# Performance work log

Hardware: AMD Instinct MI355X
Metric: run time of the kernel (lower is better)

Reference implementation:

```python
import jax, jax.numpy as jnp
import numpy as np

EPS = 1e-5

def _layernorm(x, g, b):
    mu = jnp.mean(x, axis=-1, keepdims=True)
    var = jnp.mean(jnp.square(x - mu), axis=-1, keepdims=True)
    return (x - mu) * jax.lax.rsqrt(var + EPS) * g + b

def _orthogonal(key, out_dim, in_dim):
    a = jax.random.normal(key, (max(out_dim, in_dim), min(out_dim, in_dim)), dtype=jnp.float32)
    q, r = jnp.linalg.qr(a)
    q = q * jnp.sign(jnp.diagonal(r))
    if out_dim < in_dim:
        q = q.T
    return q  # [out_dim, in_dim]

def setup_inputs() -> dict:
    key = jax.random.key(0)
    ks = jax.random.split(key, 4)
    B, OBS, H1, H2, F = 262144, 512, 128, 128, 128
    obs = jax.random.normal(ks[0], (B, OBS), dtype=jnp.float32)
    return {
        "obs": obs,
        "w1": _orthogonal(ks[1], H1, OBS), "b1": jnp.zeros((H1,), jnp.float32),
        "g1": jnp.ones((H1,), jnp.float32), "be1": jnp.zeros((H1,), jnp.float32),
        "w2": _orthogonal(ks[2], H2, H1), "b2": jnp.zeros((H2,), jnp.float32),
        "g2": jnp.ones((H2,), jnp.float32), "be2": jnp.zeros((H2,), jnp.float32),
        "w3": _orthogonal(ks[3], F, H2), "b3": jnp.zeros((F,), jnp.float32),
    }

def reference(obs, w1, b1, g1, be1, w2, b2, g2, be2, w3, b3):
    x = jnp.tanh(_layernorm(obs @ w1.T + b1, g1, be1))
    x = jnp.tanh(_layernorm(x @ w2.T + b2, g2, be2))
    return jnp.tanh(x @ w3.T + b3)
```

## Files before the change

kernel.cpp:

```cpp
#include <hip/hip_runtime.h>
#include <hip/hip_bf16.h>

typedef __attribute__((ext_vector_type(8))) __bf16 bf16x8;
typedef __attribute__((ext_vector_type(4))) float f32x4;
typedef __attribute__((ext_vector_type(8))) float f32x8;
typedef __attribute__((ext_vector_type(4))) unsigned int u32x4;

static __device__ __forceinline__ unsigned short bf16r(float f) {
  unsigned u = __builtin_bit_cast(unsigned, f);
  return (unsigned short)((u + 0x7FFFu + ((u >> 16) & 1u)) >> 16);
}

static __device__ __forceinline__ float ftanh(float x) {
  float e = __builtin_amdgcn_exp2f(x * 2.8853900817779268f);
  return 1.0f - 2.0f * __builtin_amdgcn_rcpf(e + 1.0f);
}

static __device__ __forceinline__ void gload_lds16(const void* g, void* l) {
  __builtin_amdgcn_global_load_lds(
      (const __attribute__((address_space(1))) unsigned int*)g,
      (__attribute__((address_space(3))) unsigned int*)l, 16, 0, 0);
}

__global__ void pack_kernel(const float* __restrict__ w1, const float* __restrict__ w2,
                            const float* __restrict__ w3, const float* __restrict__ b1,
                            const float* __restrict__ g1, const float* __restrict__ be1,
                            const float* __restrict__ b2, const float* __restrict__ g2,
                            const float* __restrict__ be2, const float* __restrict__ b3,
                            unsigned short* __restrict__ w1pk, unsigned short* __restrict__ w2pk,
                            unsigned short* __restrict__ w3pk, float* __restrict__ ppk) {
  int idx = blockIdx.x * 256 + threadIdx.x;
  if (idx < 65536) {
    int j = idx & 7, l = (idx >> 3) & 63, s = (idx >> 9) & 15, t = idx >> 13;
    int row = t * 16 + (l & 15);
    int col = s * 32 + (l >> 4) * 8 + j;
    w1pk[idx] = bf16r(w1[row * 512 + col]);
  } else if (idx < 81920) {
    int i = idx - 65536;
    int j = i & 7, l = (i >> 3) & 63, s = (i >> 9) & 3, t = i >> 11;
    int row = t * 16 + (l & 15);
    int col = (2 * s + (j >> 2)) * 16 + (l >> 4) * 4 + (j & 3);
    w2pk[i] = bf16r(w2[row * 128 + col]);
  } else if (idx < 98304) {
    int i = idx - 81920;
    int j = i & 7, l = (i >> 3) & 63, s = (i >> 9) & 3, t = i >> 11;
    int row = t * 16 + (l & 15);
    int col = (2 * s + (j >> 2)) * 16 + (l >> 4) * 4 + (j & 3);
    w3pk[i] = bf16r(w3[row * 128 + col]);
  } else if (idx < 99200) {
    int i = idx - 98304;
    int p = i >> 7;
    int r = i & 127;
    int qq = r >> 5, ii = r & 31;
    int m = (ii >> 2) * 16 + qq * 4 + (ii & 3);
    const float* src = (p == 0) ? b1 : (p == 1) ? g1 : (p == 2) ? be1
                     : (p == 3) ? b2 : (p == 4) ? g2 : (p == 5) ? be2 : b3;
    ppk[i] = src[m];
  }
}

__global__ __launch_bounds__(1024)
__attribute__((amdgpu_waves_per_eu(4, 4)))
void backbone_main(const float* __restrict__ obs,
                   const unsigned char* __restrict__ w1pk_g,
                   const bf16x8* __restrict__ w2pk,
                   const bf16x8* __restrict__ w3pk,
                   const float* __restrict__ ppk,
                   float* __restrict__ out) {
  __shared__ __align__(16) unsigned char w1s[131072];

  const int tid  = threadIdx.x;
  const int lane = tid & 63;
  const int wv   = tid >> 6;
  const int q    = lane >> 4;
  const int rl   = lane & 15;
  const size_t brow = (size_t)blockIdx.x * 256 + (unsigned)(wv * 16) + (unsigned)rl;

  const float* p0 = obs + brow * 512 + q * 8;

  f32x4 st[2][4];
#define LOAD_BATCH(buf, s0)                                                      \
  do {                                                                           \
    st[buf][0] = __builtin_nontemporal_load((const f32x4*)(p0 + (s0) * 32));     \
    st[buf][1] = __builtin_nontemporal_load((const f32x4*)(p0 + (s0) * 32 + 4)); \
    st[buf][2] = __builtin_nontemporal_load((const f32x4*)(p0 + (s0) * 32 + 32));\
    st[buf][3] = __builtin_nontemporal_load((const f32x4*)(p0 + (s0) * 32 + 36));\
  } while (0)

  LOAD_BATCH(0, 0);
  LOAD_BATCH(1, 2);

#pragma unroll
  for (int r = 0; r < 8; ++r) {
    gload_lds16(w1pk_g + r * 16384 + tid * 16, w1s + r * 16384 + wv * 1024);
  }
  __syncthreads();

  const bf16x8* w1l = (const bf16x8*)w1s;

  f32x4 acc[8];
#pragma unroll
  for (int t = 0; t < 8; ++t) acc[t] = (f32x4){0.f, 0.f, 0.f, 0.f};

#pragma unroll
  for (int bb = 0; bb < 8; ++bb) {
    const int cur = bb & 1;
    f32x4 a0 = st[cur][0], a1 = st[cur][1];
    f32x4 a2 = st[cur][2], a3 = st[cur][3];
    if (bb < 6) {
      LOAD_BATCH(cur, 2 * bb + 4);
    }
    f32x8 r0 = {a0.x, a0.y, a0.z, a0.w, a1.x, a1.y, a1.z, a1.w};
    f32x8 r1 = {a2.x, a2.y, a2.z, a2.w, a3.x, a3.y, a3.z, a3.w};
    bf16x8 b0 = __builtin_convertvector(r0, bf16x8);
    bf16x8 b1 = __builtin_convertvector(r1, bf16x8);
#pragma unroll
    for (int t = 0; t < 8; ++t) {
      bf16x8 af0 = w1l[(t * 16 + 2 * bb) * 64 + lane];
      acc[t] = __builtin_amdgcn_mfma_f32_16x16x32_bf16(af0, b0, acc[t], 0, 0, 0);
    }
#pragma unroll
    for (int t = 0; t < 8; ++t) {
      bf16x8 af1 = w1l[(t * 16 + 2 * bb + 1) * 64 + lane];
      acc[t] = __builtin_amdgcn_mfma_f32_16x16x32_bf16(af1, b1, acc[t], 0, 0, 0);
    }
  }
#undef LOAD_BATCH

  bf16x8 pkv[4];

  {
    const float* pb = ppk + 0 * 128 + q * 32;
    const float* pg = ppk + 1 * 128 + q * 32;
    const float* pe = ppk + 2 * 128 + q * 32;
    float s1 = 0.f, s2 = 0.f;
#pragma unroll
    for (int t = 0; t < 8; ++t) {
      f32x4 bb = *(const f32x4*)(pb + t * 4);
      f32x4 v = acc[t];
      v.x += bb.x; v.y += bb.y; v.z += bb.z; v.w += bb.w;
      acc[t] = v;
      s1 += (v.x + v.y) + (v.z + v.w);
      s2 += (v.x * v.x + v.y * v.y) + (v.z * v.z + v.w * v.w);
    }
    s1 += __shfl_xor(s1, 16, 64);
    s1 += __shfl_xor(s1, 32, 64);
    s2 += __shfl_xor(s2, 16, 64);
    s2 += __shfl_xor(s2, 32, 64);
    float mu  = s1 * (1.0f / 128.0f);
    float var = s2 * (1.0f / 128.0f) - mu * mu;
    float rs  = __builtin_amdgcn_rsqf(var + 1e-5f);
#pragma unroll
    for (int t2 = 0; t2 < 4; ++t2) {
      f32x4 ga = *(const f32x4*)(pg + (2 * t2) * 4);
      f32x4 gb = *(const f32x4*)(pg + (2 * t2 + 1) * 4);
      f32x4 ea = *(const f32x4*)(pe + (2 * t2) * 4);
      f32x4 eb = *(const f32x4*)(pe + (2 * t2 + 1) * 4);
      f32x4 va = acc[2 * t2];
      f32x4 vb = acc[2 * t2 + 1];
      f32x8 cat = {ftanh((va.x - mu) * rs * ga.x + ea.x),
                   ftanh((va.y - mu) * rs * ga.y + ea.y),
                   ftanh((va.z - mu) * rs * ga.z + ea.z),
                   ftanh((va.w - mu) * rs * ga.w + ea.w),
                   ftanh((vb.x - mu) * rs * gb.x + eb.x),
                   ftanh((vb.y - mu) * rs * gb.y + eb.y),
                   ftanh((vb.z - mu) * rs * gb.z + eb.z),
                   ftanh((vb.w - mu) * rs * gb.w + eb.w)};
      pkv[t2] = __builtin_convertvector(cat, bf16x8);
    }
  }

#pragma unroll
  for (int t = 0; t < 8; ++t) acc[t] = (f32x4){0.f, 0.f, 0.f, 0.f};
#pragma unroll
  for (int s = 0; s < 4; ++s) {
#pragma unroll
    for (int t = 0; t < 8; ++t) {
      bf16x8 af = w2pk[(t * 4 + s) * 64 + lane];
      acc[t] = __builtin_amdgcn_mfma_f32_16x16x32_bf16(af, pkv[s], acc[t], 0, 0, 0);
    }
  }

  {
    const float* pb = ppk + 3 * 128 + q * 32;
    const float* pg = ppk + 4 * 128 + q * 32;
    const float* pe = ppk + 5 * 128 + q * 32;
    float s1 = 0.f, s2 = 0.f;
#pragma unroll
    for (int t = 0; t < 8; ++t) {
      f32x4 bb = *(const f32x4*)(pb + t * 4);
      f32x4 v = acc[t];
      v.x += bb.x; v.y += bb.y; v.z += bb.z; v.w += bb.w;
      acc[t] = v;
      s1 += (v.x + v.y) + (v.z + v.w);
      s2 += (v.x * v.x + v.y * v.y) + (v.z * v.z + v.w * v.w);
    }
    s1 += __shfl_xor(s1, 16, 64);
    s1 += __shfl_xor(s1, 32, 64);
    s2 += __shfl_xor(s2, 16, 64);
    s2 += __shfl_xor(s2, 32, 64);
    float mu  = s1 * (1.0f / 128.0f);
    float var = s2 * (1.0f / 128.0f) - mu * mu;
    float rs  = __builtin_amdgcn_rsqf(var + 1e-5f);
#pragma unroll
    for (int t2 = 0; t2 < 4; ++t2) {
      f32x4 ga = *(const f32x4*)(pg + (2 * t2) * 4);
      f32x4 gb = *(const f32x4*)(pg + (2 * t2 + 1) * 4);
      f32x4 ea = *(const f32x4*)(pe + (2 * t2) * 4);
      f32x4 eb = *(const f32x4*)(pe + (2 * t2 + 1) * 4);
      f32x4 va = acc[2 * t2];
      f32x4 vb = acc[2 * t2 + 1];
      f32x8 cat = {ftanh((va.x - mu) * rs * ga.x + ea.x),
                   ftanh((va.y - mu) * rs * ga.y + ea.y),
                   ftanh((va.z - mu) * rs * ga.z + ea.z),
                   ftanh((va.w - mu) * rs * ga.w + ea.w),
                   ftanh((vb.x - mu) * rs * gb.x + eb.x),
                   ftanh((vb.y - mu) * rs * gb.y + eb.y),
                   ftanh((vb.z - mu) * rs * gb.z + eb.z),
                   ftanh((vb.w - mu) * rs * gb.w + eb.w)};
      pkv[t2] = __builtin_convertvector(cat, bf16x8);
    }
  }

#pragma unroll
  for (int t = 0; t < 8; ++t) acc[t] = (f32x4){0.f, 0.f, 0.f, 0.f};
#pragma unroll
  for (int s = 0; s < 4; ++s) {
#pragma unroll
    for (int t = 0; t < 8; ++t) {
      bf16x8 af = w3pk[(t * 4 + s) * 64 + lane];
      acc[t] = __builtin_amdgcn_mfma_f32_16x16x32_bf16(af, pkv[s], acc[t], 0, 0, 0);
    }
  }

  {
    const float* pb = ppk + 6 * 128 + q * 32;
    float* orow = out + brow * 128 + q * 4;
#pragma unroll
    for (int t = 0; t < 8; ++t) {
      f32x4 bb = *(const f32x4*)(pb + t * 4);
      f32x4 v = acc[t];
      f32x4 o = {ftanh(v.x + bb.x), ftanh(v.y + bb.y),
                 ftanh(v.z + bb.z), ftanh(v.w + bb.w)};
      __builtin_nontemporal_store(o, (f32x4*)(orow + t * 16));
    }
  }
}

extern "C" void kernel_launch(void* const* d_in, const int* in_sizes, int n_in,
                              void* d_out, int out_size, void* d_ws, size_t ws_size,
                              hipStream_t stream) {
  const float* obs = (const float*)d_in[0];
  const float* w1  = (const float*)d_in[1];
  const float* b1  = (const float*)d_in[2];
  const float* g1  = (const float*)d_in[3];
  const float* be1 = (const float*)d_in[4];
  const float* w2  = (const float*)d_in[5];
  const float* b2  = (const float*)d_in[6];
  const float* g2  = (const float*)d_in[7];
  const float* be2 = (const float*)d_in[8];
  const float* w3  = (const float*)d_in[9];
  const float* b3  = (const float*)d_in[10];

  unsigned short* w1pk = (unsigned short*)d_ws;
  unsigned short* w2pk = w1pk + 65536;
  unsigned short* w3pk = w2pk + 16384;
  float*          ppk  = (float*)(w3pk + 16384);

  pack_kernel<<<388, 256, 0, stream>>>(w1, w2, w3, b1, g1, be1, b2, g2, be2, b3,
                                       w1pk, w2pk, w3pk, ppk);

  backbone_main<<<1024, 1024, 0, stream>>>(obs, (const unsigned char*)w1pk,
                                           (const bf16x8*)w2pk, (const bf16x8*)w3pk,
                                           ppk, (float*)d_out);
}
```

Baseline: 188.1 us.

## Stage obs tiles through swizzled LDS and split W1 load into halves

Replaces register double-buffered nontemporal loads of obs with direct global-to-LDS loads into an XOR-swizzled per-wave double buffer, read back with explicit waitcnt control. W1 is now loaded into LDS in two halves (half the K range each), freeing LDS space for the obs staging. This aims to cut register pressure and improve memory-level parallelism through async LDS loads. The cost is an extra block-wide barrier and reload in the middle of the K loop, plus per-step LDS round trips and serialized waits.

```diff
diff --git a/kernel.cpp b/kernel.cpp
--- a/kernel.cpp
+++ b/kernel.cpp
@@ -4,7 +4,6 @@
 typedef __attribute__((ext_vector_type(8))) __bf16 bf16x8;
 typedef __attribute__((ext_vector_type(4))) float f32x4;
 typedef __attribute__((ext_vector_type(8))) float f32x8;
-typedef __attribute__((ext_vector_type(4))) unsigned int u32x4;
 
 static __device__ __forceinline__ unsigned short bf16r(float f) {
   unsigned u = __builtin_bit_cast(unsigned, f);
@@ -67,65 +66,90 @@
                    const bf16x8* __restrict__ w3pk,
                    const float* __restrict__ ppk,
                    float* __restrict__ out) {
-  __shared__ __align__(16) unsigned char w1s[131072];
+  __shared__ __align__(16) unsigned char lds[131072];
 
   const int tid  = threadIdx.x;
   const int lane = tid & 63;
   const int wv   = tid >> 6;
   const int q    = lane >> 4;
   const int rl   = lane & 15;
-  const size_t brow = (size_t)blockIdx.x * 256 + (unsigned)(wv * 16) + (unsigned)rl;
-
-  const float* p0 = obs + brow * 512 + q * 8;
-
-  f32x4 st[2][4];
-#define LOAD_BATCH(buf, s0)                                                      \
-  do {                                                                           \
-    st[buf][0] = __builtin_nontemporal_load((const f32x4*)(p0 + (s0) * 32));     \
-    st[buf][1] = __builtin_nontemporal_load((const f32x4*)(p0 + (s0) * 32 + 4)); \
-    st[buf][2] = __builtin_nontemporal_load((const f32x4*)(p0 + (s0) * 32 + 32));\
-    st[buf][3] = __builtin_nontemporal_load((const f32x4*)(p0 + (s0) * 32 + 36));\
-  } while (0)
-
-  LOAD_BATCH(0, 0);
-  LOAD_BATCH(1, 2);
-
-#pragma unroll
-  for (int r = 0; r < 8; ++r) {
-    gload_lds16(w1pk_g + r * 16384 + tid * 16, w1s + r * 16384 + wv * 1024);
+  const int l8   = lane >> 3;
+  const int c8   = lane & 7;
+  const unsigned rowR = blockIdx.x * 256 + wv * 16;
+  const size_t brow = (size_t)rowR + (unsigned)rl;
+
+  const unsigned char* gsrc = (const unsigned char*)obs
+      + ((size_t)rowR + (unsigned)l8) * 2048 + (unsigned)((c8 ^ l8) * 16);
+  unsigned char* obsS = lds + 65536 + wv * 4096;
+
+  const unsigned rd0 = (unsigned)(rl * 128 + ((2 * q) ^ (rl & 7)) * 16);
+  const unsigned rd1 = (unsigned)(rl * 128 + ((2 * q + 1) ^ (rl & 7)) * 16);
+
+  gload_lds16(gsrc,                 obsS);
+  gload_lds16(gsrc + 16384,         obsS + 1024);
+  gload_lds16(gsrc + 128,           obsS + 2048);
+  gload_lds16(gsrc + 128 + 16384,   obsS + 3072);
+#pragma unroll
+  for (int r = 0; r < 4; ++r) {
+    unsigned o = r * 16384 + tid * 16;
+    gload_lds16(w1pk_g + o + (o >> 13) * 8192, lds + r * 16384 + wv * 1024);
   }
   __syncthreads();
 
-  const bf16x8* w1l = (const bf16x8*)w1s;
+  const bf16x8* w1l = (const bf16x8*)lds;
 
   f32x4 acc[8];
 #pragma unroll
   for (int t = 0; t < 8; ++t) acc[t] = (f32x4){0.f, 0.f, 0.f, 0.f};
 
-#pragma unroll
-  for (int bb = 0; bb < 8; ++bb) {
-    const int cur = bb & 1;
-    f32x4 a0 = st[cur][0], a1 = st[cur][1];
-    f32x4 a2 = st[cur][2], a3 = st[cur][3];
-    if (bb < 6) {
-      LOAD_BATCH(cur, 2 * bb + 4);
-    }
-    f32x8 r0 = {a0.x, a0.y, a0.z, a0.w, a1.x, a1.y, a1.z, a1.w};
-    f32x8 r1 = {a2.x, a2.y, a2.z, a2.w, a3.x, a3.y, a3.z, a3.w};
-    bf16x8 b0 = __builtin_convertvector(r0, bf16x8);
-    bf16x8 b1 = __builtin_convertvector(r1, bf16x8);
-#pragma unroll
-    for (int t = 0; t < 8; ++t) {
-      bf16x8 af0 = w1l[(t * 16 + 2 * bb) * 64 + lane];
-      acc[t] = __builtin_amdgcn_mfma_f32_16x16x32_bf16(af0, b0, acc[t], 0, 0, 0);
-    }
-#pragma unroll
-    for (int t = 0; t < 8; ++t) {
-      bf16x8 af1 = w1l[(t * 16 + 2 * bb + 1) * 64 + lane];
-      acc[t] = __builtin_amdgcn_mfma_f32_16x16x32_bf16(af1, b1, acc[t], 0, 0, 0);
-    }
-  }
-#undef LOAD_BATCH
+#define KSTEP(s, WAITSTR)                                                        \
+  {                                                                              \
+    asm volatile("s_waitcnt " WAITSTR ::: "memory");                             \
+    __builtin_amdgcn_sched_barrier(0);                                           \
+    unsigned char* slot = obsS + ((s) & 1) * 2048;                               \
+    f32x4 r0 = *(const f32x4*)(slot + rd0);                                      \
+    f32x4 r1 = *(const f32x4*)(slot + rd1);                                      \
+    asm volatile("s_waitcnt lgkmcnt(0)" ::: "memory");                           \
+    __builtin_amdgcn_sched_barrier(0);                                           \
+    if ((s) + 2 <= 15) {                                                         \
+      gload_lds16(gsrc + ((s) + 2) * 128,         slot);                         \
+      gload_lds16(gsrc + ((s) + 2) * 128 + 16384, slot + 1024);                  \
+    }                                                                            \
+    f32x8 rr = {r0.x, r0.y, r0.z, r0.w, r1.x, r1.y, r1.z, r1.w};                 \
+    bf16x8 bfrag = __builtin_convertvector(rr, bf16x8);                          \
+    _Pragma("unroll")                                                            \
+    for (int t = 0; t < 8; ++t) {                                                \
+      bf16x8 af = w1l[(t * 8 + ((s) & 7)) * 64 + lane];                          \
+      acc[t] = __builtin_amdgcn_mfma_f32_16x16x32_bf16(af, bfrag, acc[t], 0, 0, 0); \
+    }                                                                            \
+  }
+
+  KSTEP(0, "vmcnt(2)")
+  KSTEP(1, "vmcnt(2)")
+  KSTEP(2, "vmcnt(2)")
+  KSTEP(3, "vmcnt(2)")
+  KSTEP(4, "vmcnt(2)")
+  KSTEP(5, "vmcnt(2)")
+  KSTEP(6, "vmcnt(2)")
+  KSTEP(7, "vmcnt(2)")
+
+  __syncthreads();
+#pragma unroll
+  for (int r = 0; r < 4; ++r) {
+    unsigned o = r * 16384 + tid * 16;
+    gload_lds16(w1pk_g + o + ((o >> 13) + 1) * 8192, lds + r * 16384 + wv * 1024);
+  }
+  __syncthreads();
+
+  KSTEP(8,  "vmcnt(2)")
+  KSTEP(9,  "vmcnt(2)")
+  KSTEP(10, "vmcnt(2)")
+  KSTEP(11, "vmcnt(2)")
+  KSTEP(12, "vmcnt(2)")
+  KSTEP(13, "vmcnt(2)")
+  KSTEP(14, "vmcnt(2)")
+  KSTEP(15, "vmcnt(0)")
+#undef KSTEP
 
   bf16x8 pkv[4];
 
```

New measurement: 198.6 us. +5.6%, slower.
